# Kernel tuning notes

Hardware: AMD Instinct MI355X
Metric: run time of the kernel (lower is better)

Reference implementation:

```python
import jax, jax.numpy as jnp
import numpy as np

B, S, L = 512, 150, 50          # batch, history length, prediction horizon
D, H, FF, NL = 128, 8, 256, 2   # d_model, heads, ffn hidden, encoder layers
DT = 0.1                        # self.dt


def _layernorm(x, g, b, eps=1e-5):
    mu = jnp.mean(x, axis=-1, keepdims=True)
    var = jnp.mean((x - mu) ** 2, axis=-1, keepdims=True)
    return (x - mu) / jnp.sqrt(var + eps) * g + b


def setup_inputs() -> dict:
    key = jax.random.key(0)
    ks = jax.random.split(key, 16)
    # inputs[:, :, :] = (position y, speed v, gap s, delta_v) over history
    pos = 100.0 * jax.random.uniform(ks[0], (B, S), jnp.float32)
    vel = 5.0 + 20.0 * jax.random.uniform(ks[1], (B, S), jnp.float32)
    gap = 10.0 + 30.0 * jax.random.uniform(ks[2], (B, S), jnp.float32)
    dvel = 0.5 * jax.random.normal(ks[3], (B, S), jnp.float32)
    inputs = jnp.stack([pos, vel, gap, dvel], axis=-1)
    # his_labels: leader position / speed over the horizon; keep leader ahead
    lead_y = inputs[:, -1, 0:1] + inputs[:, -1, 2:3] + 15.0 * jnp.arange(1, L + 1, dtype=jnp.float32)[None, :]
    lead_v = 15.0 + 2.0 * jax.random.uniform(ks[4], (B, L), jnp.float32)
    his_labels = jnp.stack([lead_y, lead_v], axis=-1)

    def u(k, shape, scale=0.05):
        return scale * jax.random.normal(k, shape, jnp.float32)

    params = dict(
        emb_w=u(ks[5], (D, 1)), emb_b=jnp.zeros((D,), jnp.float32),
        ipw=u(ks[6], (NL, 3 * D, D)), ipb=jnp.zeros((NL, 3 * D), jnp.float32),
        opw=u(ks[7], (NL, D, D)), opb=jnp.zeros((NL, D), jnp.float32),
        ln1g=jnp.ones((NL, D), jnp.float32), ln1b=jnp.zeros((NL, D), jnp.float32),
        l1w=u(ks[8], (NL, FF, D)), l1b=jnp.zeros((NL, FF), jnp.float32),
        l2w=u(ks[9], (NL, D, FF)), l2b=jnp.zeros((NL, D), jnp.float32),
        ln2g=jnp.ones((NL, D), jnp.float32), ln2b=jnp.zeros((NL, D), jnp.float32),
        dec_w=u(ks[10], (1, D)), dec_b=jnp.zeros((1,), jnp.float32),
        fus_w=u(ks[11], (1, 3)), fus_b=jnp.zeros((1,), jnp.float32),
    )
    return dict(inputs=inputs, his_labels=his_labels,
                s_0_input=jnp.float32(2.0), T_input=jnp.float32(1.5),
                a_input=jnp.float32(1.0), b_input=jnp.float32(1.5),
                v_d_input=jnp.float32(30.0), **params)


def _encoder_layer(x, mask, ipw, ipb, opw, opb, ln1g, ln1b, l1w, l1b, l2w, l2b, ln2g, ln2b):
    # x: [S, B, D]; torch post-norm TransformerEncoderLayer, relu, dropout=0
    Sq, Bb, Dd = x.shape
    dh = Dd // H
    qkv = x @ ipw.T + ipb                       # [S, B, 3D]
    q, k, v = jnp.split(qkv, 3, axis=-1)

    def heads(t):                               # [S, B, D] -> [B, H, S, dh]
        return t.reshape(Sq, Bb, H, dh).transpose(1, 2, 0, 3)

    q, k, v = heads(q), heads(k), heads(v)
    scores = jnp.einsum('bhqd,bhkd->bhqk', q, k) / jnp.sqrt(jnp.float32(dh)) + mask
    attn = jax.nn.softmax(scores, axis=-1)
    o = jnp.einsum('bhqk,bhkd->bhqd', attn, v).transpose(2, 0, 1, 3).reshape(Sq, Bb, Dd)
    o = o @ opw.T + opb
    x = _layernorm(x + o, ln1g, ln1b)
    ff = jax.nn.relu(x @ l1w.T + l1b) @ l2w.T + l2b
    return _layernorm(x + ff, ln2g, ln2b)


def _idm(inp_last, his, s0, T, a, b, vd, dt):
    # inp_last: [B, 4] = (y, v, s, delta_v); his: [B, L, 2] leader (y, v)
    y, v, s, dv = inp_last[:, 0], inp_last[:, 1], inp_last[:, 2], inp_last[:, 3]
    sq = 2.0 * jnp.sqrt(a * b)
    s_x = s0 + jnp.maximum(0.0, v * T + v * dv / sq)
    a_f = a * (1.0 - (v / vd) ** 4 - (s_x / s) ** 2)
    v0 = jnp.maximum(v + a_f * dt, 0.0)
    # NOTE: faithful to the torch source's bug: after the clipping loop the
    # loop variable i == B-1, so y_pred[:,0,0] = y + v_pred[B-1,0,0]*dt uses
    # the LAST batch element's speed for every row.
    y0 = y + v0[-1] * dt

    def step(carry, his_j):
        vj, yj = carry
        dvj = his_j[:, 1] - vj
        sj = his_j[:, 0] - yj
        sx = s0 + jnp.maximum(0.0, vj * T + vj * dvj / sq)
        acc = a * (1.0 - (vj / vd) ** 4 - (sx / sj) ** 2)
        v2 = vj + acc * dt
        v2 = jnp.where(v2 <= 0.0, 0.0, v2)
        y2 = yj + v2 * dt
        return (v2, y2), y2

    _, ys = jax.lax.scan(step, (v0, y0), his[:, :L - 1].transpose(1, 0, 2))  # ys: [L-1, B]
    y_pred = jnp.concatenate([y0[:, None], ys.T], axis=1)  # [B, L]
    return y_pred[:, :, None]


def reference(inputs, his_labels, s_0_input, T_input, a_input, b_input, v_d_input,
              emb_w, emb_b, ipw, ipb, opw, opb, ln1g, ln1b,
              l1w, l1b, l2w, l2b, ln2g, ln2b, dec_w, dec_b, fus_w, fus_b):
    src_in = inputs[:, :, 0:1]                               # [B, S, 1]
    src = src_in.transpose(1, 0, 2) @ emb_w.T + emb_b       # [S, B, D]
    mask = jnp.where(jnp.tril(jnp.ones((S, S), bool)), 0.0, -jnp.inf).astype(src.dtype)
    x = src
    for l in range(NL):
        x = _encoder_layer(x, mask, ipw[l], ipb[l], opw[l], opb[l],
                           ln1g[l], ln1b[l], l1w[l], l1b[l],
                           l2w[l], l2b[l], ln2g[l], ln2b[l])
    enc = x[-1]                                              # [B, D]
    out = jnp.broadcast_to(enc, (L, B, D)) @ dec_w.T + dec_b  # [L, B, 1]
    out = out.transpose(1, 0, 2)                             # [B, L, 1]
    # hist: per-row linspace(last, last + dv*L, L+1)[1:] == last + dv*(1..L)
    last = src_in[:, -1, 0]
    dvh = (last - src_in[:, -(1 + L), 0]) / L
    hist = (last[:, None] + dvh[:, None] * jnp.arange(1, L + 1, dtype=last.dtype))[:, :, None]
    y_idm = _idm(inputs[:, -1, :], his_labels, s_0_input, T_input,
                 a_input, b_input, v_d_input, DT)
    fusion = jnp.concatenate([out, hist, y_idm], axis=2)     # [B, L, 3]
    return fusion @ fus_w.T + fus_b                          # [B, L, 1]
```

## Files before the change

kernel.cpp:

```cpp
#include <hip/hip_runtime.h>

#define BB   512
#define SS   150
#define LL   50
#define DD   128
#define HH   8
#define DHH  16
#define FFD  256
#define NLL  2
#define MM   (SS*BB)
#define MDSZ ((size_t)MM*DD)
#define HREG 2400
#define MLAST 76288

typedef unsigned short u16;
typedef __attribute__((ext_vector_type(8))) short short8;
typedef __attribute__((ext_vector_type(4))) float f32x4;

__device__ __forceinline__ float bf2f(u16 u) {
    return __uint_as_float(((unsigned int)u) << 16);
}
__device__ __forceinline__ u16 f2bf(float f) {
    unsigned int x = __float_as_uint(f);
    unsigned int r = (x + 0x7fffu + ((x >> 16) & 1u)) >> 16;
    return (u16)r;
}
__device__ __forceinline__ float ldv(const void* p, size_t i, int bf) {
    return bf ? bf2f(((const u16*)p)[i]) : ((const float*)p)[i];
}
__device__ __forceinline__ float rd_scalar(const void* p) {
    const u16* q = (const u16*)p;
    u16 lo = q[0];
    if (lo != 0) return bf2f(lo);
    return *(const float*)p;
}
__device__ __forceinline__ f32x4 mfma16(short8 a, short8 b, f32x4 c) {
    return __builtin_amdgcn_mfma_f32_16x16x32_bf16(a, b, c, 0, 0, 0);
}
__device__ __forceinline__ float fexp2(float x) {
#if __has_builtin(__builtin_amdgcn_exp2f)
    return __builtin_amdgcn_exp2f(x);
#else
    return exp2f(x);
#endif
}
__device__ __forceinline__ float frcp(float x) {
#if __has_builtin(__builtin_amdgcn_rcpf)
    return __builtin_amdgcn_rcpf(x);
#else
    return 1.f / x;
#endif
}

__global__ void detect_kernel(const u16* __restrict__ ln1g, int* __restrict__ flag)
{
    *flag = (ln1g[0] == 0x3F80) ? 1 : 0;
}

#define WOFF_IPW 0
#define WOFF_OPW 98304
#define WOFF_L1W 131072
#define WOFF_L2W 196608
#define WTOTAL   262144
__global__ __launch_bounds__(256) void prep_kernel(
    const void* __restrict__ ipw, const void* __restrict__ opw,
    const void* __restrict__ l1w, const void* __restrict__ l2w,
    u16* __restrict__ wbf, const int* __restrict__ flag)
{
    int bf = *flag;
    int idx = blockIdx.x * 256 + threadIdx.x;
    if (idx >= WTOTAL) return;
    const void* src; size_t i;
    if (idx < WOFF_OPW)      { src = ipw; i = idx; }
    else if (idx < WOFF_L1W) { src = opw; i = idx - WOFF_OPW; }
    else if (idx < WOFF_L2W) { src = l1w; i = idx - WOFF_L1W; }
    else                     { src = l2w; i = idx - WOFF_L2W; }
    wbf[idx] = bf ? ((const u16*)src)[i] : f2bf(((const float*)src)[i]);
}

__global__ void prep2_kernel(
    const void* __restrict__ ipw, const void* __restrict__ ipb,
    const void* __restrict__ emb_w, const void* __restrict__ emb_b,
    float* __restrict__ uw, const int* __restrict__ flag)
{
    int bf = *flag;
    int c = threadIdx.x;
    float su = 0.f, sw = 0.f;
    for (int k = 0; k < DD; ++k) {
        float wv = ldv(ipw, (size_t)c * DD + k, bf);
        su += wv * ldv(emb_w, k, bf);
        sw += wv * ldv(emb_b, k, bf);
    }
    uw[c]       = su;
    uw[384 + c] = sw + ldv(ipb, c, bf);
}

__global__ __launch_bounds__(192) void attn0_kernel(
    const void* __restrict__ inputs, const float* __restrict__ uw,
    u16* __restrict__ o, const int* __restrict__ flag)
{
    __shared__ float pos_s[SS];
    __shared__ float pmax_s[SS];
    __shared__ float pmin_s[SS];

    int bid = blockIdx.x;
    int h = bid & 7, b = bid >> 3;
    int tid = threadIdx.x;
    int bf = *flag;

    if (tid < SS) pos_s[tid] = ldv(inputs, (size_t)(b * SS + tid) * 4 + 0, bf);
    __syncthreads();
    if (tid == 0) {
        float mx = pos_s[0], mn = pos_s[0];
        pmax_s[0] = mx; pmin_s[0] = mn;
        for (int t = 1; t < SS; ++t) {
            mx = fmaxf(mx, pos_s[t]); mn = fminf(mn, pos_s[t]);
            pmax_s[t] = mx; pmin_s[t] = mn;
        }
    }

    const float* uq = uw + h * 16;
    const float* wq = uw + 384 + h * 16;
    const float* uk = uw + 128 + h * 16;
    float A = 0.f, Bc = 0.f;
#pragma unroll
    for (int d = 0; d < 16; ++d) { A += uq[d] * uk[d]; Bc += wq[d] * uk[d]; }
    __syncthreads();

    int q = tid;
    if (q >= SS) return;
    float pq  = pos_s[q];
    const float L2E = 1.4426950408889634f;
    float cql = 0.25f * (pq * A + Bc) * L2E;
    float Ml  = fmaxf(cql * pmax_s[q], cql * pmin_s[q]);
    float s = 0.f, wsum = 0.f;
    for (int t = 0; t <= q; ++t) {
        float pt = pos_s[t];
        float e = fexp2(__builtin_fmaf(cql, pt, -Ml));
        s += e; wsum += e * pt;
    }
    float mq = wsum * frcp(s);

    const float* uv = uw + 256 + h * 16;
    const float* wv = uw + 384 + 256 + h * 16;
    u16 ov[16];
#pragma unroll
    for (int d = 0; d < 16; ++d) ov[d] = f2bf(mq * uv[d] + wv[d]);
    u16* dst = o + ((size_t)q * BB + b) * DD + h * DHH;
    *(uint4*)(dst)     = *(uint4*)(ov);
    *(uint4*)(dst + 8) = *(uint4*)(ov + 8);
}

#define LDPK 72
template<int EPI>
__global__ __launch_bounds__(256) void mfma_gemm(
    const u16* __restrict__ A, const u16* __restrict__ W,
    const void* __restrict__ bias, size_t boff,
    void* __restrict__ out, const u16* __restrict__ resid,
    int N, int K, const int* __restrict__ flag,
    const void* __restrict__ lng, const void* __restrict__ lnb, size_t goff,
    const void* __restrict__ ew, const void* __restrict__ eb,
    int madd, int nadd)
{
    __shared__ __attribute__((aligned(16))) u16 As[64 * LDPK];
    __shared__ __attribute__((aligned(16))) u16 Bs[128 * LDPK];

    int bf = *flag;
    int tid  = threadIdx.x;
    int wave = tid >> 6, lane = tid & 63;
    int wy = wave >> 1, wx = wave & 1;
    int quad = lane >> 4, lr = lane & 15;
    int m0 = blockIdx.x * 64, n0 = (blockIdx.y + nadd) * 128;

    int aR = tid >> 2,          aC = (tid & 3) * 16;
    int bR0 = tid >> 2,         bC0 = (tid & 3) * 16;
    int bR1 = (tid + 256) >> 2, bC1 = (tid & 3) * 16;

    f32x4 acc[2][4] = {};

    for (int k0 = 0; k0 < K; k0 += 64) {
        const u16* ap  = A + (size_t)(m0 + aR) * K + k0 + aC;
        const u16* wp0 = W + (size_t)(n0 + bR0) * K + k0 + bC0;
        const u16* wp1 = W + (size_t)(n0 + bR1) * K + k0 + bC1;
        uint4 av0 = *(const uint4*)(ap);
        uint4 av1 = *(const uint4*)(ap + 8);
        uint4 w00 = *(const uint4*)(wp0);
        uint4 w01 = *(const uint4*)(wp0 + 8);
        uint4 w10 = *(const uint4*)(wp1);
        uint4 w11 = *(const uint4*)(wp1 + 8);
        __syncthreads();
        *(uint4*)(As + aR * LDPK + aC)       = av0;
        *(uint4*)(As + aR * LDPK + aC + 8)   = av1;
        *(uint4*)(Bs + bR0 * LDPK + bC0)     = w00;
        *(uint4*)(Bs + bR0 * LDPK + bC0 + 8) = w01;
        *(uint4*)(Bs + bR1 * LDPK + bC1)     = w10;
        *(uint4*)(Bs + bR1 * LDPK + bC1 + 8) = w11;
        __syncthreads();

#pragma unroll
        for (int ks = 0; ks < 64; ks += 32) {
            short8 a[2], b[4];
#pragma unroll
            for (int i = 0; i < 2; ++i)
                a[i] = *(const short8*)(As + (wy * 32 + i * 16 + lr) * LDPK + ks + quad * 8);
#pragma unroll
            for (int j = 0; j < 4; ++j)
                b[j] = *(const short8*)(Bs + (wx * 64 + j * 16 + lr) * LDPK + ks + quad * 8);
#pragma unroll
            for (int i = 0; i < 2; ++i)
#pragma unroll
                for (int j = 0; j < 4; ++j)
                    acc[i][j] = mfma16(a[i], b[j], acc[i][j]);
        }
    }

    if (EPI == 3 || EPI == 4) {
        float bvj[4];
#pragma unroll
        for (int j = 0; j < 4; ++j) bvj[j] = ldv(bias, boff + wx * 64 + j * 16 + lr, bf);

        float ewj[4], ebj[4], posr[2][4];
        if (EPI == 4) {
            int sblk  = m0 >> 9;
            int bbase = m0 & 511;
#pragma unroll
            for (int j = 0; j < 4; ++j) {
                int c = wx * 64 + j * 16 + lr;
                ewj[j] = ldv(ew, c, bf);
                ebj[j] = ldv(eb, c, bf);
            }
#pragma unroll
            for (int i = 0; i < 2; ++i)
#pragma unroll
                for (int r = 0; r < 4; ++r) {
                    int b = bbase + wy * 32 + i * 16 + quad * 4 + r;
                    posr[i][r] = ldv((const void*)resid, (size_t)(b * SS + sblk) * 4 + 0, bf);
                }
        }

        float s1[2][4] = {}, s2[2][4] = {};
#pragma unroll
        for (int j = 0; j < 4; ++j) {
            int c = wx * 64 + j * 16 + lr;
#pragma unroll
            for (int i = 0; i < 2; ++i)
#pragma unroll
                for (int r = 0; r < 4; ++r) {
                    int m = m0 + wy * 32 + i * 16 + quad * 4 + r;
                    float rv = (EPI == 4)
                               ? __builtin_fmaf(posr[i][r], ewj[j], ebj[j])
                               : bf2f(resid[(size_t)m * 128 + c]);
                    float v = acc[i][j][r] + bvj[j] + rv;
                    acc[i][j][r] = v;
                    s1[i][r] += v;
                    s2[i][r] += v * v;
                }
        }
#pragma unroll
        for (int i = 0; i < 2; ++i)
#pragma unroll
            for (int r = 0; r < 4; ++r)
#pragma unroll
                for (int msk = 1; msk < 16; msk <<= 1) {
                    s1[i][r] += __shfl_xor(s1[i][r], msk);
                    s2[i][r] += __shfl_xor(s2[i][r], msk);
                }

        __syncthreads();
        float* red = (float*)As;
        if (lr == 0) {
#pragma unroll
            for (int i = 0; i < 2; ++i)
#pragma unroll
                for (int r = 0; r < 4; ++r) {
                    int row = wy * 32 + i * 16 + quad * 4 + r;
                    red[wx * 128 + row]      = s1[i][r];
                    red[wx * 128 + 64 + row] = s2[i][r];
                }
        }
        __syncthreads();

        float gj[4], bj[4];
#pragma unroll
        for (int j = 0; j < 4; ++j) {
            int c = wx * 64 + j * 16 + lr;
            gj[j] = ldv(lng, goff + c, bf);
            bj[j] = ldv(lnb, goff + c, bf);
        }
#pragma unroll
        for (int i = 0; i < 2; ++i)
#pragma unroll
            for (int r = 0; r < 4; ++r) {
                int row = wy * 32 + i * 16 + quad * 4 + r;
                float t1 = red[row] + red[128 + row];
                float t2 = red[64 + row] + red[192 + row];
                float mu = t1 * (1.f / 128.f);
                float rstd = rsqrtf(t2 * (1.f / 128.f) - mu * mu + 1e-5f);
                size_t m = (size_t)(m0 + row);
#pragma unroll
                for (int j = 0; j < 4; ++j) {
                    int c = wx * 64 + j * 16 + lr;
                    ((u16*)out)[m * 128 + c] =
                        f2bf((acc[i][j][r] - mu) * rstd * gj[j] + bj[j]);
                }
            }
        return;
    }

    if (EPI == 2) {
        int mglob = m0 + madd;
        int sblk  = mglob >> 9;
        int bbase = mglob & 511;
#pragma unroll
        for (int j = 0; j < 4; ++j) {
            int c = n0 + wx * 64 + j * 16 + lr;
            float bvj = ldv(bias, boff + c, bf);
            int part = c >> 7;
            int hh   = (c >> 4) & 7;
#pragma unroll
            for (int i = 0; i < 2; ++i) {
#pragma unroll
                for (int r = 0; r < 4; ++r) {
                    int brow = bbase + wy * 32 + i * 16 + quad * 4 + r;
                    float v = acc[i][j][r] + bvj;
                    ((u16*)out)[((size_t)(brow * 8 + hh) * 3 + part) * HREG
                                + sblk * 16 + lr] = f2bf(v);
                }
            }
        }
        return;
    }

#pragma unroll
    for (int j = 0; j < 4; ++j) {
        int c = n0 + wx * 64 + j * 16 + lr;
        float bvj = ldv(bias, boff + c, bf);
#pragma unroll
        for (int i = 0; i < 2; ++i) {
#pragma unroll
            for (int r = 0; r < 4; ++r) {
                int m = m0 + wy * 32 + i * 16 + quad * 4 + r;
                float v = acc[i][j][r] + bvj;
                if (EPI == 1) v = fmaxf(v, 0.f);
                ((u16*)out)[(size_t)m * N + c] = f2bf(v);
            }
        }
    }
}

__global__ __launch_bounds__(64) void attn1_kernel(
    const u16* __restrict__ qkv, u16* __restrict__ o1)
{
    int bid = blockIdx.x;
    int h = bid & 7, b = bid >> 3;
    int lane = threadIdx.x;
    const u16* qbase = qkv + (size_t)bid * 3 * HREG;
    const u16* kbase = qbase + HREG;
    const u16* vbase = qbase + 2 * HREG;

    float qv[16];
    {
        uint4 q0 = *(const uint4*)(qbase + 149 * 16);
        uint4 q1 = *(const uint4*)(qbase + 149 * 16 + 8);
        const unsigned int* qw = (const unsigned int*)&q0;
#pragma unroll
        for (int i = 0; i < 4; ++i) {
            qv[2 * i]     = bf2f((u16)(qw[i] & 0xffff));
            qv[2 * i + 1] = bf2f((u16)(qw[i] >> 16));
        }
        qw = (const unsigned int*)&q1;
#pragma unroll
        for (int i = 0; i < 4; ++i) {
            qv[8 + 2 * i]     = bf2f((u16)(qw[i] & 0xffff));
            qv[8 + 2 * i + 1] = bf2f((u16)(qw[i] >> 16));
        }
    }

    const float Cs = 0.36067376022224085f;
    float s = 0.f;
    float ov[16] = {};
    for (int t = lane; t < SS; t += 64) {
        uint4 k0 = *(const uint4*)(kbase + t * 16);
        uint4 k1 = *(const uint4*)(kbase + t * 16 + 8);
        float dot = 0.f;
        const unsigned int* kw = (const unsigned int*)&k0;
#pragma unroll
        for (int i = 0; i < 4; ++i) {
            dot = __builtin_fmaf(qv[2 * i],     bf2f((u16)(kw[i] & 0xffff)), dot);
            dot = __builtin_fmaf(qv[2 * i + 1], bf2f((u16)(kw[i] >> 16)),    dot);
        }
        kw = (const unsigned int*)&k1;
#pragma unroll
        for (int i = 0; i < 4; ++i) {
            dot = __builtin_fmaf(qv[8 + 2 * i],     bf2f((u16)(kw[i] & 0xffff)), dot);
            dot = __builtin_fmaf(qv[8 + 2 * i + 1], bf2f((u16)(kw[i] >> 16)),    dot);
        }
        float e = fexp2(dot * Cs);
        s += e;
        uint4 v0 = *(const uint4*)(vbase + t * 16);
        uint4 v1 = *(const uint4*)(vbase + t * 16 + 8);
        const unsigned int* vw = (const unsigned int*)&v0;
#pragma unroll
        for (int i = 0; i < 4; ++i) {
            ov[2 * i]     = __builtin_fmaf(e, bf2f((u16)(vw[i] & 0xffff)), ov[2 * i]);
            ov[2 * i + 1] = __builtin_fmaf(e, bf2f((u16)(vw[i] >> 16)),    ov[2 * i + 1]);
        }
        vw = (const unsigned int*)&v1;
#pragma unroll
        for (int i = 0; i < 4; ++i) {
            ov[8 + 2 * i]     = __builtin_fmaf(e, bf2f((u16)(vw[i] & 0xffff)), ov[8 + 2 * i]);
            ov[8 + 2 * i + 1] = __builtin_fmaf(e, bf2f((u16)(vw[i] >> 16)),    ov[8 + 2 * i + 1]);
        }
    }
#pragma unroll
    for (int msk = 1; msk < 64; msk <<= 1) {
        s += __shfl_xor(s, msk);
#pragma unroll
        for (int d = 0; d < 16; ++d) ov[d] += __shfl_xor(ov[d], msk);
    }
    float inv = frcp(s);
    if (lane < 16)
        o1[(size_t)b * 128 + h * 16 + lane] = f2bf(ov[lane] * inv);
}

__global__ __launch_bounds__(64) void head_kernel(
    const u16* __restrict__ xlast, const void* __restrict__ inputs,
    const void* __restrict__ his,
    const void* s0p, const void* Tp, const void* ap, const void* bp, const void* vdp,
    const void* __restrict__ dec_w, const void* dec_b,
    const void* fus_w, const void* fus_b,
    void* __restrict__ out, const int* __restrict__ flag)
{
    int bf = *flag;
    int b = blockIdx.x * 64 + threadIdx.x;
    if (b >= BB) return;

    const u16* enc = xlast + (size_t)b * DD;
    float dot = 0.f;
    for (int d = 0; d < DD; ++d) dot += bf2f(enc[d]) * ldv(dec_w, d, bf);
    float outv = dot + ldv(dec_b, 0, bf);

    float last = ldv(inputs, (size_t)(b * SS + (SS - 1)) * 4 + 0, bf);
    float prev = ldv(inputs, (size_t)(b * SS + (SS - 1 - LL)) * 4 + 0, bf);
    float dvh = (last - prev) * (1.f / (float)LL);

    float s0 = rd_scalar(s0p), T = rd_scalar(Tp), a = rd_scalar(ap);
    float bb = rd_scalar(bp), vd = rd_scalar(vdp);
    float sq = 2.f * sqrtf(a * bb);
    const float dt = 0.1f;

    auto v0compute = [&](int bi) {
        size_t ip = (size_t)(bi * SS + (SS - 1)) * 4;
        float v  = ldv(inputs, ip + 1, bf);
        float s  = ldv(inputs, ip + 2, bf);
        float dv = ldv(inputs, ip + 3, bf);
        float sx = s0 + fmaxf(0.f, v * T + v * dv / sq);
        float r = v / vd, r2 = r * r;
        float rs = sx / s;
        float af = a * (1.f - r2 * r2 - rs * rs);
        return fmaxf(v + af * dt, 0.f);
    };
    float v0_last = v0compute(BB - 1);
    float v0      = v0compute(b);
    float y0 = last + v0_last * dt;

    float fw0 = ldv(fus_w, 0, bf), fw1 = ldv(fus_w, 1, bf), fw2 = ldv(fus_w, 2, bf);
    float fb  = ldv(fus_b, 0, bf);

    auto store = [&](int idx, float val) {
        if (bf) ((u16*)out)[idx] = f2bf(val);
        else    ((float*)out)[idx] = val;
    };

    store(b * LL + 0, fw0 * outv + fw1 * (last + dvh * 1.f) + fw2 * y0 + fb);

    float vj = v0, yj = y0;
    for (int j = 0; j < LL - 1; ++j) {
        float hy = ldv(his, (size_t)(b * LL + j) * 2 + 0, bf);
        float hv = ldv(his, (size_t)(b * LL + j) * 2 + 1, bf);
        float dvj = hv - vj;
        float sj  = hy - yj;
        float sx = s0 + fmaxf(0.f, vj * T + vj * dvj / sq);
        float r = vj / vd, r2 = r * r;
        float rs = sx / sj;
        float acc = a * (1.f - r2 * r2 - rs * rs);
        float v2 = vj + acc * dt;
        v2 = (v2 <= 0.f) ? 0.f : v2;
        float y2 = yj + v2 * dt;
        int l = j + 1;
        float histl = last + dvh * (float)(l + 1);
        store(b * LL + l, fw0 * outv + fw1 * histl + fw2 * y2 + fb);
        vj = v2; yj = y2;
    }
}

extern "C" void kernel_launch(void* const* d_in, const int* in_sizes, int n_in,
                              void* d_out, int out_size, void* d_ws, size_t ws_size,
                              hipStream_t stream)
{
    const void* inputs = d_in[0];
    const void* his    = d_in[1];
    const void* s0p    = d_in[2];
    const void* Tp     = d_in[3];
    const void* ap     = d_in[4];
    const void* bp     = d_in[5];
    const void* vdp    = d_in[6];
    const void* emb_w  = d_in[7];
    const void* emb_b  = d_in[8];
    const void* ipw    = d_in[9];
    const void* ipb    = d_in[10];
    const void* opw    = d_in[11];
    const void* opb    = d_in[12];
    const void* ln1g   = d_in[13];
    const void* ln1b   = d_in[14];
    const void* l1w    = d_in[15];
    const void* l1b    = d_in[16];
    const void* l2w    = d_in[17];
    const void* l2b    = d_in[18];
    const void* ln2g   = d_in[19];
    const void* ln2b   = d_in[20];
    const void* dec_w  = d_in[21];
    const void* dec_b  = d_in[22];
    const void* fus_w  = d_in[23];
    const void* fus_b  = d_in[24];

    u16*   wsu  = (u16*)d_ws;
    u16*   bx   = wsu;
    u16*   bqkv = wsu + 1 * MDSZ;
    u16*   bo   = wsu + 4 * MDSZ;
    u16*   h1   = wsu + 5 * MDSZ;
    u16*   wbf  = wsu + 7 * MDSZ;
    int*   flag = (int*)(wsu + 7 * MDSZ + WTOTAL);
    float* uw   = (float*)(wsu + 7 * MDSZ + WTOTAL + 2);
    u16*   o1   = bo;
    u16*   y1   = bo + 512 * 128;
    u16*   z1   = bo + 2 * 512 * 128;

    detect_kernel<<<1, 1, 0, stream>>>((const u16*)ln1g, flag);
    prep_kernel<<<(WTOTAL + 255) / 256, 256, 0, stream>>>(ipw, opw, l1w, l2w, wbf, flag);
    prep2_kernel<<<1, 384, 0, stream>>>(ipw, ipb, emb_w, emb_b, uw, flag);

    attn0_kernel<<<BB * HH, 192, 0, stream>>>(inputs, uw, bo, flag);
    mfma_gemm<4><<<dim3(MM / 64, 1), 256, 0, stream>>>(
        bo, wbf + WOFF_OPW, opb, 0,
        bx, (const u16*)inputs, 128, 128, flag, ln1g, ln1b, 0,
        emb_w, emb_b, 0, 0);
    mfma_gemm<1><<<dim3(MM / 64, 2), 256, 0, stream>>>(
        bx, wbf + WOFF_L1W, l1b, 0,
        h1, nullptr, 256, 128, flag, nullptr, nullptr, 0,
        nullptr, nullptr, 0, 0);
    mfma_gemm<3><<<dim3(MM / 64, 1), 256, 0, stream>>>(
        h1, wbf + WOFF_L2W, l2b, 0,
        bx, bx, 128, 256, flag, ln2g, ln2b, 0,
        nullptr, nullptr, 0, 0);

    mfma_gemm<2><<<dim3(MM / 64, 2), 256, 0, stream>>>(
        bx, wbf + WOFF_IPW + (size_t)384 * 128, ipb, 384,
        bqkv, nullptr, 384, 128, flag, nullptr, nullptr, 0,
        nullptr, nullptr, 0, 1);
    mfma_gemm<2><<<dim3(512 / 64, 1), 256, 0, stream>>>(
        bx + (size_t)MLAST * 128, wbf + WOFF_IPW + (size_t)384 * 128, ipb, 384,
        bqkv, nullptr, 384, 128, flag, nullptr, nullptr, 0,
        nullptr, nullptr, MLAST, 0);
    attn1_kernel<<<BB * HH, 64, 0, stream>>>(bqkv, o1);
    mfma_gemm<3><<<dim3(512 / 64, 1), 256, 0, stream>>>(
        o1, wbf + WOFF_OPW + (size_t)128 * 128, opb, 128,
        y1, bx + (size_t)MLAST * 128, 128, 128, flag, ln1g, ln1b, 128,
        nullptr, nullptr, 0, 0);
    mfma_gemm<1><<<dim3(512 / 64, 2), 256, 0, stream>>>(
        y1, wbf + WOFF_L1W + (size_t)256 * 128, l1b, 256,
        h1, nullptr, 256, 128, flag, nullptr, nullptr, 0,
        nullptr, nullptr, 0, 0);
    mfma_gemm<3><<<dim3(512 / 64, 1), 256, 0, stream>>>(
        h1, wbf + WOFF_L2W + (size_t)128 * 256, l2b, 128,
        z1, y1, 128, 256, flag, ln2g, ln2b, 128,
        nullptr, nullptr, 0, 0);

    head_kernel<<<BB / 64, 64, 0, stream>>>(
        z1, inputs, his, s0p, Tp, ap, bp, vdp,
        dec_w, dec_b, fus_w, fus_b, d_out, flag);

    (void)in_sizes; (void)n_in; (void)out_size; (void)ws_size;
}
```

Before: 297.1 us.

## Fold last-layer K/V projections into per-batch query-side attention kernel

The last encoder layer only needs attention output for the final query position. Instead of projecting K and V for all 76800 tokens with a large GEMM, the new attention kernel uses associativity. It projects the query through Wk to get a per-head vector qt, scores raw inputs against it, takes an exp-weighted sum of the raw inputs, and then applies Wv once. This removes a large GEMM and its QKV buffer traffic, in exchange for scalar-FMA work per batch element with only 512 blocks and heavy shared-memory use.

```diff
diff --git a/kernel.cpp b/kernel.cpp
--- a/kernel.cpp
+++ b/kernel.cpp
@@ -10,7 +10,6 @@
 #define NLL  2
 #define MM   (SS*BB)
 #define MDSZ ((size_t)MM*DD)
-#define HREG 2400
 #define MLAST 76288
 
 typedef unsigned short u16;
@@ -159,8 +158,7 @@
     void* __restrict__ out, const u16* __restrict__ resid,
     int N, int K, const int* __restrict__ flag,
     const void* __restrict__ lng, const void* __restrict__ lnb, size_t goff,
-    const void* __restrict__ ew, const void* __restrict__ eb,
-    int madd, int nadd)
+    const void* __restrict__ ew, const void* __restrict__ eb)
 {
     __shared__ __attribute__((aligned(16))) u16 As[64 * LDPK];
     __shared__ __attribute__((aligned(16))) u16 Bs[128 * LDPK];
@@ -170,7 +168,7 @@
     int wave = tid >> 6, lane = tid & 63;
     int wy = wave >> 1, wx = wave & 1;
     int quad = lane >> 4, lr = lane & 15;
-    int m0 = blockIdx.x * 64, n0 = (blockIdx.y + nadd) * 128;
+    int m0 = blockIdx.x * 64, n0 = blockIdx.y * 128;
 
     int aR = tid >> 2,          aC = (tid & 3) * 16;
     int bR0 = tid >> 2,         bC0 = (tid & 3) * 16;
@@ -307,30 +305,6 @@
         return;
     }
 
-    if (EPI == 2) {
-        int mglob = m0 + madd;
-        int sblk  = mglob >> 9;
-        int bbase = mglob & 511;
-#pragma unroll
-        for (int j = 0; j < 4; ++j) {
-            int c = n0 + wx * 64 + j * 16 + lr;
-            float bvj = ldv(bias, boff + c, bf);
-            int part = c >> 7;
-            int hh   = (c >> 4) & 7;
-#pragma unroll
-            for (int i = 0; i < 2; ++i) {
-#pragma unroll
-                for (int r = 0; r < 4; ++r) {
-                    int brow = bbase + wy * 32 + i * 16 + quad * 4 + r;
-                    float v = acc[i][j][r] + bvj;
-                    ((u16*)out)[((size_t)(brow * 8 + hh) * 3 + part) * HREG
-                                + sblk * 16 + lr] = f2bf(v);
-                }
-            }
-        }
-        return;
-    }
-
 #pragma unroll
     for (int j = 0; j < 4; ++j) {
         int c = n0 + wx * 64 + j * 16 + lr;
@@ -348,79 +322,113 @@
     }
 }
 
-__global__ __launch_bounds__(64) void attn1_kernel(
-    const u16* __restrict__ qkv, u16* __restrict__ o1)
-{
-    int bid = blockIdx.x;
-    int h = bid & 7, b = bid >> 3;
-    int lane = threadIdx.x;
-    const u16* qbase = qkv + (size_t)bid * 3 * HREG;
-    const u16* kbase = qbase + HREG;
-    const u16* vbase = qbase + 2 * HREG;
-
-    float qv[16];
-    {
-        uint4 q0 = *(const uint4*)(qbase + 149 * 16);
-        uint4 q1 = *(const uint4*)(qbase + 149 * 16 + 8);
-        const unsigned int* qw = (const unsigned int*)&q0;
-#pragma unroll
-        for (int i = 0; i < 4; ++i) {
-            qv[2 * i]     = bf2f((u16)(qw[i] & 0xffff));
-            qv[2 * i + 1] = bf2f((u16)(qw[i] >> 16));
-        }
-        qw = (const unsigned int*)&q1;
-#pragma unroll
-        for (int i = 0; i < 4; ++i) {
-            qv[8 + 2 * i]     = bf2f((u16)(qw[i] & 0xffff));
-            qv[8 + 2 * i + 1] = bf2f((u16)(qw[i] >> 16));
-        }
-    }
+__global__ __launch_bounds__(256) void attn1_kernel(
+    const u16* __restrict__ bx, const u16* __restrict__ w1,
+    const void* __restrict__ ipb, u16* __restrict__ o1, const int* __restrict__ flag)
+{
+    __shared__ __attribute__((aligned(16))) u16 X[SS * 128];
+    __shared__ float qv[128];
+    __shared__ float qt[8][132];
+    __shared__ float cb_s[8];
+    __shared__ float E[SS][8];
+    __shared__ float ssum[8];
+
+    int bf = *flag;
+    int b = blockIdx.x;
+    int tid = threadIdx.x;
+
+    for (int idx = tid; idx < SS * 16; idx += 256) {
+        int row = idx >> 4, ch = idx & 15;
+        *(uint4*)(X + row * 128 + ch * 8) =
+            *(const uint4*)(bx + ((size_t)(row * 512 + b)) * 128 + ch * 8);
+    }
+    __syncthreads();
+
+    if (tid < 128) {
+        const u16* wr = w1 + (size_t)tid * 128;
+        float acc = 0.f;
+        for (int kc = 0; kc < 16; ++kc) {
+            short8 wv = *(const short8*)(wr + kc * 8);
+            short8 xv = *(const short8*)(X + 149 * 128 + kc * 8);
+#pragma unroll
+            for (int i = 0; i < 8; ++i)
+                acc = __builtin_fmaf(bf2f((u16)wv[i]), bf2f((u16)xv[i]), acc);
+        }
+        qv[tid] = acc + ldv(ipb, 384 + tid, bf);
+    }
+    __syncthreads();
+
+    for (int o = tid; o < 1024; o += 256) {
+        int h = o >> 7, k = o & 127;
+        float acc = 0.f;
+#pragma unroll
+        for (int d = 0; d < 16; ++d)
+            acc = __builtin_fmaf(bf2f(w1[(size_t)(128 + h * 16 + d) * 128 + k]),
+                                 qv[h * 16 + d], acc);
+        qt[h][k] = acc;
+    }
+    if (tid < 8) {
+        float acc = 0.f;
+#pragma unroll
+        for (int d = 0; d < 16; ++d)
+            acc = __builtin_fmaf(qv[tid * 16 + d],
+                                 ldv(ipb, 384 + 128 + tid * 16 + d, bf), acc);
+        cb_s[tid] = acc;
+    }
+    __syncthreads();
 
     const float Cs = 0.36067376022224085f;
-    float s = 0.f;
-    float ov[16] = {};
-    for (int t = lane; t < SS; t += 64) {
-        uint4 k0 = *(const uint4*)(kbase + t * 16);
-        uint4 k1 = *(const uint4*)(kbase + t * 16 + 8);
-        float dot = 0.f;
-        const unsigned int* kw = (const unsigned int*)&k0;
-#pragma unroll
-        for (int i = 0; i < 4; ++i) {
-            dot = __builtin_fmaf(qv[2 * i],     bf2f((u16)(kw[i] & 0xffff)), dot);
-            dot = __builtin_fmaf(qv[2 * i + 1], bf2f((u16)(kw[i] >> 16)),    dot);
-        }
-        kw = (const unsigned int*)&k1;
-#pragma unroll
-        for (int i = 0; i < 4; ++i) {
-            dot = __builtin_fmaf(qv[8 + 2 * i],     bf2f((u16)(kw[i] & 0xffff)), dot);
-            dot = __builtin_fmaf(qv[8 + 2 * i + 1], bf2f((u16)(kw[i] >> 16)),    dot);
-        }
-        float e = fexp2(dot * Cs);
-        s += e;
-        uint4 v0 = *(const uint4*)(vbase + t * 16);
-        uint4 v1 = *(const uint4*)(vbase + t * 16 + 8);
-        const unsigned int* vw = (const unsigned int*)&v0;
-#pragma unroll
-        for (int i = 0; i < 4; ++i) {
-            ov[2 * i]     = __builtin_fmaf(e, bf2f((u16)(vw[i] & 0xffff)), ov[2 * i]);
-            ov[2 * i + 1] = __builtin_fmaf(e, bf2f((u16)(vw[i] >> 16)),    ov[2 * i + 1]);
-        }
-        vw = (const unsigned int*)&v1;
-#pragma unroll
-        for (int i = 0; i < 4; ++i) {
-            ov[8 + 2 * i]     = __builtin_fmaf(e, bf2f((u16)(vw[i] & 0xffff)), ov[8 + 2 * i]);
-            ov[8 + 2 * i + 1] = __builtin_fmaf(e, bf2f((u16)(vw[i] >> 16)),    ov[8 + 2 * i + 1]);
-        }
-    }
-#pragma unroll
-    for (int msk = 1; msk < 64; msk <<= 1) {
-        s += __shfl_xor(s, msk);
-#pragma unroll
-        for (int d = 0; d < 16; ++d) ov[d] += __shfl_xor(ov[d], msk);
-    }
-    float inv = frcp(s);
-    if (lane < 16)
-        o1[(size_t)b * 128 + h * 16 + lane] = f2bf(ov[lane] * inv);
+    for (int o = tid; o < SS * 8; o += 256) {
+        int t = o >> 3, h = o & 7;
+        float acc = 0.f;
+        for (int kc = 0; kc < 16; ++kc) {
+            short8 xv = *(const short8*)(X + t * 128 + kc * 8);
+#pragma unroll
+            for (int i = 0; i < 8; ++i)
+                acc = __builtin_fmaf(qt[h][kc * 8 + i], bf2f((u16)xv[i]), acc);
+        }
+        E[t][h] = fexp2((acc + cb_s[h]) * Cs);
+    }
+    __syncthreads();
+
+    if (tid < 128) {
+        int h = tid >> 4, j = tid & 15;
+        float acc = 0.f;
+        for (int t = j; t < SS; t += 16) acc += E[t][h];
+#pragma unroll
+        for (int m = 1; m < 16; m <<= 1) acc += __shfl_xor(acc, m);
+        if (j == 0) ssum[h] = acc;
+    }
+    __syncthreads();
+
+    if (tid < 128) {
+        int h = tid >> 4, k0 = (tid & 15) * 8;
+        float wacc[8] = {};
+        for (int t = 0; t < SS; ++t) {
+            float e = E[t][h];
+            short8 xv = *(const short8*)(X + t * 128 + k0);
+#pragma unroll
+            for (int i = 0; i < 8; ++i)
+                wacc[i] = __builtin_fmaf(e, bf2f((u16)xv[i]), wacc[i]);
+        }
+#pragma unroll
+        for (int i = 0; i < 8; ++i) qt[h][k0 + i] = wacc[i];
+    }
+    __syncthreads();
+
+    if (tid < 128) {
+        int h = tid >> 4;
+        const u16* wr = w1 + (size_t)(256 + tid) * 128;
+        float acc = 0.f;
+        for (int kc = 0; kc < 16; ++kc) {
+            short8 wv = *(const short8*)(wr + kc * 8);
+#pragma unroll
+            for (int i = 0; i < 8; ++i)
+                acc = __builtin_fmaf(bf2f((u16)wv[i]), qt[h][kc * 8 + i], acc);
+        }
+        o1[(size_t)b * 128 + tid] =
+            f2bf(acc * frcp(ssum[tid >> 4]) + ldv(ipb, 384 + 256 + tid, bf));
+    }
 }
 
 __global__ __launch_bounds__(64) void head_kernel(
@@ -526,7 +534,6 @@
 
     u16*   wsu  = (u16*)d_ws;
     u16*   bx   = wsu;
-    u16*   bqkv = wsu + 1 * MDSZ;
     u16*   bo   = wsu + 4 * MDSZ;
     u16*   h1   = wsu + 5 * MDSZ;
     u16*   wbf  = wsu + 7 * MDSZ;
@@ -544,37 +551,30 @@
     mfma_gemm<4><<<dim3(MM / 64, 1), 256, 0, stream>>>(
         bo, wbf + WOFF_OPW, opb, 0,
         bx, (const u16*)inputs, 128, 128, flag, ln1g, ln1b, 0,
-        emb_w, emb_b, 0, 0);
+        emb_w, emb_b);
     mfma_gemm<1><<<dim3(MM / 64, 2), 256, 0, stream>>>(
         bx, wbf + WOFF_L1W, l1b, 0,
         h1, nullptr, 256, 128, flag, nullptr, nullptr, 0,
-        nullptr, nullptr, 0, 0);
+        nullptr, nullptr);
     mfma_gemm<3><<<dim3(MM / 64, 1), 256, 0, stream>>>(
         h1, wbf + WOFF_L2W, l2b, 0,
         bx, bx, 128, 256, flag, ln2g, ln2b, 0,
-        nullptr, nullptr, 0, 0);
-
-    mfma_gemm<2><<<dim3(MM / 64, 2), 256, 0, stream>>>(
-        bx, wbf + WOFF_IPW + (size_t)384 * 128, ipb, 384,
-        bqkv, nullptr, 384, 128, flag, nullptr, nullptr, 0,
-        nullptr, nullptr, 0, 1);
-    mfma_gemm<2><<<dim3(512 / 64, 1), 256, 0, stream>>>(
-        bx + (size_t)MLAST * 128, wbf + WOFF_IPW + (size_t)384 * 128, ipb, 384,
-        bqkv, nullptr, 384, 128, flag, nullptr, nullptr, 0,
-        nullptr, nullptr, MLAST, 0);
-    attn1_kernel<<<BB * HH, 64, 0, stream>>>(bqkv, o1);
+        nullptr, nullptr);
+
+    attn1_kernel<<<BB, 256, 0, stream>>>(
+        bx, wbf + WOFF_IPW + (size_t)384 * 128, ipb, o1, flag);
     mfma_gemm<3><<<dim3(512 / 64, 1), 256, 0, stream>>>(
         o1, wbf + WOFF_OPW + (size_t)128 * 128, opb, 128,
         y1, bx + (size_t)MLAST * 128, 128, 128, flag, ln1g, ln1b, 128,
-        nullptr, nullptr, 0, 0);
+        nullptr, nullptr);
     mfma_gemm<1><<<dim3(512 / 64, 2), 256, 0, stream>>>(
         y1, wbf + WOFF_L1W + (size_t)256 * 128, l1b, 256,
         h1, nullptr, 256, 128, flag, nullptr, nullptr, 0,
-        nullptr, nullptr, 0, 0);
+        nullptr, nullptr);
     mfma_gemm<3><<<dim3(512 / 64, 1), 256, 0, stream>>>(
         h1, wbf + WOFF_L2W + (size_t)128 * 256, l2b, 128,
         z1, y1, 128, 256, flag, ln2g, ln2b, 128,
-        nullptr, nullptr, 0, 0);
+        nullptr, nullptr);
 
     head_kernel<<<BB / 64, 64, 0, stream>>>(
         z1, inputs, his, s0p, Tp, ap, bp, vdp,
```

Measured after the change: 285.8 us, median of 3. 1.04x faster.
